# Performance work log

Measured on AMD Instinct MI355X. Metric: run time of the kernel, lower is better.

Reference implementation:

```python
import jax, jax.numpy as jnp
import numpy as np

NUM_HEADS = 8
EPS = 1e-12  # torch F.normalize eps


def _l2norm(t):
    # F.normalize(t, dim=-1): t / max(||t||, eps)
    n = jnp.sqrt(jnp.sum(t * t, axis=-1, keepdims=True))
    return t / jnp.maximum(n, EPS)


def setup_inputs() -> dict:
    key = jax.random.key(0)
    ks = jax.random.split(key, 4)
    B, C, H, W = 16, 384, 32, 32
    x = jax.random.normal(ks[0], (B, C, H, W), dtype=jnp.float32)
    temperature = jnp.ones((NUM_HEADS, 1, 1), dtype=jnp.float32)
    qkv_w = jax.random.normal(ks[1], (3 * C, C), dtype=jnp.float32) * (1.0 / np.sqrt(C))
    qkv_b = jnp.zeros((3 * C,), dtype=jnp.float32)
    proj_w = jax.random.normal(ks[2], (C, C), dtype=jnp.float32) * (1.0 / np.sqrt(C))
    proj_b = jnp.zeros((C,), dtype=jnp.float32)
    return {"x": x, "temperature": temperature, "qkv_w": qkv_w,
            "qkv_b": qkv_b, "proj_w": proj_w, "proj_b": proj_b}


def reference(x, temperature, qkv_w, qkv_b, proj_w, proj_b):
    B, C, H, W = x.shape
    nH = NUM_HEADS
    hd = C // nH
    N = H * W
    x_flat = x.reshape(B, C, N).transpose(0, 2, 1)            # [B, N, C]
    qkv = x_flat @ qkv_w.T + qkv_b                             # [B, N, 3C]
    qkv = qkv.reshape(B, N, 3, nH, hd).transpose(2, 0, 3, 1, 4)  # [3, B, nH, N, hd]
    q, k, v = qkv[0], qkv[1], qkv[2]
    q = _l2norm(q)
    k = _l2norm(k)
    attn = jnp.einsum('bhnd,bhmd->bhnm', q, k) * temperature   # [B, nH, N, N]
    attn = jax.nn.softmax(attn, axis=-1)
    out = jnp.einsum('bhnm,bhmd->bhnd', attn, v)               # [B, nH, N, hd]
    out = out.transpose(0, 2, 1, 3).reshape(B, N, C)           # [B, N, C]
    out = out @ proj_w.T + proj_b
    return out.transpose(0, 2, 1).reshape(B, C, H, W)
```

## Files before the change

kernel.cpp:

```cpp
#include <hip/hip_runtime.h>
#include <hip/hip_bf16.h>

#define Bb   16
#define Cc   384
#define Nn   1024
#define NH   8
#define HD   48
#define C3   1152
#define D64  64

typedef _Float16 f16x8 __attribute__((ext_vector_type(8)));
typedef __fp16   h16x2 __attribute__((ext_vector_type(2)));
typedef float    f32x4 __attribute__((ext_vector_type(4)));
typedef unsigned short ushort8 __attribute__((ext_vector_type(8)));

__device__ inline unsigned short f2h(float f) {
  union { _Float16 h; unsigned short u; } cv;
  cv.h = (_Float16)f;
  return cv.u;
}
__device__ inline unsigned int pk2u(float a, float b) {
  union { h16x2 v; unsigned int u; } cv;
  cv.v = __builtin_amdgcn_cvt_pkrtz(a, b);
  return cv.u;
}
__device__ inline void plswap(unsigned int &a, unsigned int &b) {
  asm("v_permlane16_swap_b32 %0, %1" : "+v"(a), "+v"(b));
}
__device__ inline f16x8 mk8(unsigned int a, unsigned int b,
                            unsigned int c, unsigned int d) {
  union { unsigned int u[4]; f16x8 h; } cv;
  cv.u[0] = a; cv.u[1] = b; cv.u[2] = c; cv.u[3] = d;
  return cv.h;
}

__device__ inline void gload_lds16(const unsigned short* g, unsigned short* l) {
  __builtin_amdgcn_global_load_lds(
      (const __attribute__((address_space(1))) void*)g,
      (__attribute__((address_space(3))) void*)l, 16, 0, 0);
}

__global__ __launch_bounds__(256) void prep_xsplit_kernel(
    const float* __restrict__ qkv_w, const float* __restrict__ pw,
    const float* __restrict__ x,
    unsigned short* __restrict__ wqh, unsigned short* __restrict__ pwh,
    unsigned short* __restrict__ vt, unsigned short* __restrict__ xh) {
  __shared__ float tile[64][65];
  const int bid = blockIdx.x;
  if (bid < 1728) {
    int i = bid * 256 + threadIdx.x;
    wqh[i] = f2h(qkv_w[i]);
  } else if (bid < 2304) {
    int i = (bid - 1728) * 256 + threadIdx.x;
    pwh[i] = f2h(pw[i]);
  } else if (bid < 3328) {
    int idx8 = (bid - 2304) * 256 + threadIdx.x;
    int bh = idx8 >> 11;
    int rem = idx8 & 2047;
    int row = 48 + (rem >> 7);
    int col = (rem & 127) * 8;
    unsigned short fill = (row == 48) ? (unsigned short)0x3C00 : (unsigned short)0;
    ushort8 v;
#pragma unroll
    for (int j = 0; j < 8; j++) v[j] = fill;
    *(ushort8*)(vt + (size_t)bh * D64 * Nn + (size_t)row * Nn + col) = v;
  } else {
    const int xb = bid - 3328;
    const int b  = xb / 96;
    const int rem = xb % 96;
    const int c0 = (rem / 16) * 64;
    const int n0 = (rem % 16) * 64;
    const int t  = threadIdx.x;
    const int rl = t >> 2, sc = (t & 3) * 16;
    {
      const float* src = x + ((size_t)b * Cc + c0 + rl) * Nn + n0 + sc;
#pragma unroll
      for (int i = 0; i < 4; i++) {
        float4 v = *(const float4*)(src + i * 4);
        tile[rl][sc + i * 4 + 0] = v.x; tile[rl][sc + i * 4 + 1] = v.y;
        tile[rl][sc + i * 4 + 2] = v.z; tile[rl][sc + i * 4 + 3] = v.w;
      }
    }
    __syncthreads();
    {
      ushort8 h0, h1;
#pragma unroll
      for (int i = 0; i < 8; i++) h0[i] = f2h(tile[sc + i][rl]);
#pragma unroll
      for (int i = 0; i < 8; i++) h1[i] = f2h(tile[sc + 8 + i][rl]);
      size_t dst = ((size_t)b * Nn + n0 + rl) * Cc + c0 + sc;
      *(ushort8*)(xh + dst) = h0; *(ushort8*)(xh + dst + 8) = h1;
    }
  }
}

__global__ __launch_bounds__(256, 4) void qkv_mfma(
    const unsigned short* __restrict__ wh,
    const unsigned short* __restrict__ xh,
    const float* __restrict__ bias, const float* __restrict__ temp,
    unsigned short* __restrict__ qh, unsigned short* __restrict__ kh,
    unsigned short* __restrict__ vt) {
  __shared__ unsigned short lds[128 * 136];
  unsigned short* Ash = lds;
  unsigned short* Bsh = lds + 6144;

  const int b  = blockIdx.z;
  const int yb = blockIdx.y;
  const int j0 = yb * 96;
  const int n0 = blockIdx.x * 128;
  const int tid = threadIdx.x;
  const int wave = tid >> 6, lane = tid & 63;
  const int quad = lane >> 4, l16 = lane & 15;
  const int wm = (wave >> 1) * 48, wn = (wave & 1) * 64;
  const int hs = wave >> 1;

  f32x4 acc[3][4];
#pragma unroll
  for (int mi = 0; mi < 3; mi++)
#pragma unroll
    for (int ni = 0; ni < 4; ni++) acc[mi][ni] = (f32x4){0.f, 0.f, 0.f, 0.f};

  const int sw = l16 & 7;

  for (int c0 = 0; c0 < Cc; c0 += 64) {
    __syncthreads();
#pragma unroll
    for (int s = 0; s < 3; s++) {
      int r  = s * 32 + wave * 8 + (lane >> 3);
      int cg = ((lane & 7) ^ (lane >> 3)) * 8;
      gload_lds16(wh + (size_t)(j0 + r) * Cc + c0 + cg,
                  &Ash[(s * 32 + wave * 8) * 64]);
    }
#pragma unroll
    for (int s = 0; s < 4; s++) {
      int r  = s * 32 + wave * 8 + (lane >> 3);
      int cg = ((lane & 7) ^ (lane >> 3)) * 8;
      gload_lds16(xh + ((size_t)b * Nn + n0 + r) * Cc + c0 + cg,
                  &Bsh[(s * 32 + wave * 8) * 64]);
    }
    __syncthreads();

#pragma unroll
    for (int ks = 0; ks < 64; ks += 32) {
      const int ach = (((ks >> 3) + quad) ^ sw) * 8;
      f16x8 ah[3], bh[4];
#pragma unroll
      for (int mi = 0; mi < 3; mi++)
        ah[mi] = *(const f16x8*)&Ash[(wm + mi * 16 + l16) * 64 + ach];
#pragma unroll
      for (int ni = 0; ni < 4; ni++)
        bh[ni] = *(const f16x8*)&Bsh[(wn + ni * 16 + l16) * 64 + ach];
#pragma unroll
      for (int mi = 0; mi < 3; mi++)
#pragma unroll
        for (int ni = 0; ni < 4; ni++)
          acc[mi][ni] = __builtin_amdgcn_mfma_f32_16x16x32_f16(ah[mi], bh[ni], acc[mi][ni], 0, 0, 0);
    }
  }

  const int part = yb >> 2;
  const int tq   = yb & 3;
  float bv[3][4];
#pragma unroll
  for (int mi = 0; mi < 3; mi++)
#pragma unroll
    for (int r = 0; r < 4; r++)
      bv[mi][r] = bias[j0 + wm + mi * 16 + quad * 4 + r];

  if (part < 2) {
    unsigned short* dst = part ? kh : qh;
    const float tmul = part ? 1.0f : temp[2 * tq + hs] * 1.44269504f;
    __syncthreads();
#pragma unroll
    for (int ni = 0; ni < 4; ni++) {
      float vals[3][4];
      float ss = 0.f;
#pragma unroll
      for (int mi = 0; mi < 3; mi++)
#pragma unroll
        for (int r = 0; r < 4; r++) {
          float v = acc[mi][ni][r] + bv[mi][r];
          vals[mi][r] = v; ss += v * v;
        }
      ss += __shfl_xor(ss, 16);
      ss += __shfl_xor(ss, 32);
      float scale = tmul / fmaxf(sqrtf(ss), 1e-12f);
      int n = wn + ni * 16 + l16;
#pragma unroll
      for (int mi = 0; mi < 3; mi++) {
        ushort4 sv;
        sv.x = f2h(vals[mi][0] * scale);
        sv.y = f2h(vals[mi][1] * scale);
        sv.z = f2h(vals[mi][2] * scale);
        sv.w = f2h(vals[mi][3] * scale);
        *(ushort4*)&lds[n * 136 + hs * 64 + mi * 16 + quad * 4] = sv;
      }
    }
    {
      int n = tid >> 1, h2 = tid & 1;
      ushort8 z = {0, 0, 0, 0, 0, 0, 0, 0};
      *(ushort8*)&lds[n * 136 + h2 * 64 + 48] = z;
      *(ushort8*)&lds[n * 136 + h2 * 64 + 56] = z;
    }
    __syncthreads();
#pragma unroll
    for (int it = 0; it < 8; it++) {
      int n = wave * 32 + it * 4 + (lane >> 4);
      int chunk = lane & 15;
      int hs3 = chunk >> 3, c8 = (chunk & 7) * 8;
      int h = 2 * tq + hs3;
      ushort8 v = *(const ushort8*)&lds[n * 136 + hs3 * 64 + c8];
      *(ushort8*)(dst + ((size_t)(b * NH + h) * Nn + n0 + n) * D64 + c8) = v;
    }
  } else {
    const int h = 2 * tq + hs;
#pragma unroll
    for (int mi = 0; mi < 3; mi++) {
#pragma unroll
      for (int r = 0; r < 4; r++) {
        int d = mi * 16 + quad * 4 + r;
        unsigned short* vrow = vt + ((size_t)(b * NH + h) * D64 + d) * Nn;
#pragma unroll
        for (int ni = 0; ni < 4; ni++) {
          int n = n0 + wn + ni * 16 + l16;
          vrow[n] = f2h(acc[mi][ni][r] + bv[mi][r]);
        }
      }
    }
  }
}

__global__ __launch_bounds__(256, 4) void attn_mfma(
    const unsigned short* __restrict__ qh, const unsigned short* __restrict__ kh,
    const unsigned short* __restrict__ vt,
    unsigned short* __restrict__ obh) {
  __shared__ __align__(16) unsigned short Kt[2][64 * 64];
  __shared__ __align__(16) unsigned short Vt[2][64 * 64];

  const int bid = blockIdx.x;
  const int hb = bid & 127;
  const int q0 = (bid >> 7) * 128;
  const int b = hb >> 3, h = hb & 7;
  const int tid = threadIdx.x;
  const int wave = tid >> 6, lane = tid & 63;
  const int quad = lane >> 4, l16 = lane & 15;
  const int qsw = ((quad & 1) << 1) | (quad >> 1);
  const int sx = (l16 & 7) * 8;

  const size_t headQ = ((size_t)(b * NH + h) * Nn) * D64;
  const unsigned short* Qg = qh + headQ + (size_t)(q0 + wave * 32) * D64;
  const unsigned short* Kg = kh + headQ;
  const unsigned short* Vg = vt + ((size_t)(b * NH + h) * D64) * Nn;

  f16x8 qa0[2], qa1[2];
#pragma unroll
  for (int m = 0; m < 2; m++) {
    qa0[m] = *(const f16x8*)(Qg + (m * 16 + l16) * D64 + quad * 8);
    qa1[m] = *(const f16x8*)(Qg + (m * 16 + l16) * D64 + quad * 8 + 32);
  }

  f32x4 oacc[2][4];
#pragma unroll
  for (int m = 0; m < 2; m++)
#pragma unroll
    for (int g = 0; g < 4; g++) oacc[m][g] = (f32x4){0.f, 0.f, 0.f, 0.f};
  const f32x4 zf = (f32x4){0.f, 0.f, 0.f, 0.f};

  const int srow = lane >> 3;
  const int scol = ((lane & 7) ^ srow) * 8;
  const int r0 = wave * 16;
  const unsigned short* KgS = Kg + (size_t)(r0 + srow) * D64 + scol;
  const unsigned short* VgS = Vg + (size_t)(r0 + srow) * Nn + scol;

  gload_lds16(KgS,           &Kt[0][r0 * 64]);
  gload_lds16(KgS + 8 * D64, &Kt[0][(r0 + 8) * 64]);
  gload_lds16(VgS,           &Vt[0][r0 * 64]);
  gload_lds16(VgS + 8 * Nn,  &Vt[0][(r0 + 8) * 64]);

  for (int kt = 0; kt < Nn / 64; kt++) {
    __syncthreads();
    const int cur = kt & 1;
    if (kt < Nn / 64 - 1) {
      const unsigned short* kn = KgS + (size_t)(kt + 1) * 64 * D64;
      const unsigned short* vn = VgS + (size_t)(kt + 1) * 64;
      gload_lds16(kn,           &Kt[cur ^ 1][r0 * 64]);
      gload_lds16(kn + 8 * D64, &Kt[cur ^ 1][(r0 + 8) * 64]);
      gload_lds16(vn,           &Vt[cur ^ 1][r0 * 64]);
      gload_lds16(vn + 8 * Nn,  &Vt[cur ^ 1][(r0 + 8) * 64]);
    }
    const unsigned short* Kl = Kt[cur];
    const unsigned short* Vl = Vt[cur];

    f32x4 sT[2][4];
    __builtin_amdgcn_s_setprio(1);
#pragma unroll
    for (int g = 0; g < 4; g++) {
      const unsigned short* kb = Kl + (g * 16 + l16) * 64;
      const int go = (quad * 8) ^ sx;
      f16x8 kf0 = *(const f16x8*)&kb[go];
      f16x8 kf1 = *(const f16x8*)&kb[go ^ 32];
#pragma unroll
      for (int m = 0; m < 2; m++) {
        f32x4 s = __builtin_amdgcn_mfma_f32_16x16x32_f16(kf0, qa0[m], zf, 0, 0, 0);
        sT[m][g] = __builtin_amdgcn_mfma_f32_16x16x32_f16(kf1, qa1[m], s, 0, 0, 0);
      }
    }
    __builtin_amdgcn_s_setprio(0);

    unsigned int w0[2][4], w1[2][4];
#pragma unroll
    for (int m = 0; m < 2; m++)
#pragma unroll
      for (int g = 0; g < 4; g++) {
        float e0 = __builtin_amdgcn_exp2f(sT[m][g][0]);
        float e1 = __builtin_amdgcn_exp2f(sT[m][g][1]);
        float e2 = __builtin_amdgcn_exp2f(sT[m][g][2]);
        float e3 = __builtin_amdgcn_exp2f(sT[m][g][3]);
        w0[m][g] = pk2u(e0, e1);
        w1[m][g] = pk2u(e2, e3);
      }

    f16x8 pa[2][2];
#pragma unroll
    for (int m = 0; m < 2; m++) {
      plswap(w0[m][0], w0[m][1]);
      plswap(w1[m][0], w1[m][1]);
      plswap(w0[m][2], w0[m][3]);
      plswap(w1[m][2], w1[m][3]);
      pa[m][0] = mk8(w0[m][0], w1[m][0], w0[m][1], w1[m][1]);
      pa[m][1] = mk8(w0[m][2], w1[m][2], w0[m][3], w1[m][3]);
    }

    __builtin_amdgcn_s_setprio(1);
#pragma unroll
    for (int g = 0; g < 4; g++) {
      const unsigned short* vb = Vl + (g * 16 + l16) * 64;
      const int go = (qsw * 8) ^ sx;
      f16x8 vf0 = *(const f16x8*)&vb[go];
      f16x8 vf1 = *(const f16x8*)&vb[go ^ 32];
#pragma unroll
      for (int m = 0; m < 2; m++) {
        oacc[m][g] = __builtin_amdgcn_mfma_f32_16x16x32_f16(vf0, pa[m][0], oacc[m][g], 0, 0, 0);
        oacc[m][g] = __builtin_amdgcn_mfma_f32_16x16x32_f16(vf1, pa[m][1], oacc[m][g], 0, 0, 0);
      }
    }
    __builtin_amdgcn_s_setprio(0);
  }

#pragma unroll
  for (int m = 0; m < 2; m++) {
    float inv = __builtin_amdgcn_rcpf(__shfl(oacc[m][3][0], l16));
    size_t obase = ((size_t)b * Nn + q0 + wave * 32 + m * 16 + l16) * Cc + h * HD;
#pragma unroll
    for (int g = 0; g < 3; g++) {
      ushort4 sv;
      sv.x = f2h(oacc[m][g][0] * inv);
      sv.y = f2h(oacc[m][g][1] * inv);
      sv.z = f2h(oacc[m][g][2] * inv);
      sv.w = f2h(oacc[m][g][3] * inv);
      *(ushort4*)(obh + obase + g * 16 + quad * 4) = sv;
    }
  }
}

__global__ __launch_bounds__(256, 4) void proj_mfma(
    const unsigned short* __restrict__ pwh,
    const unsigned short* __restrict__ obh,
    const float* __restrict__ pb, float* __restrict__ out) {
  __shared__ unsigned short Ash[128 * 64];
  __shared__ unsigned short Bsh[128 * 64];
  const int b  = blockIdx.z;
  const int c0m = blockIdx.y * 128;
  const int n0 = blockIdx.x * 128;
  const int tid = threadIdx.x;
  const int wave = tid >> 6, lane = tid & 63;
  const int quad = lane >> 4, l16 = lane & 15;
  const int wm = (wave >> 1) * 64, wn = (wave & 1) * 64;

  f32x4 acc[4][4];
#pragma unroll
  for (int mi = 0; mi < 4; mi++)
#pragma unroll
    for (int ni = 0; ni < 4; ni++) acc[mi][ni] = (f32x4){0.f, 0.f, 0.f, 0.f};

  const int sw = l16 & 7;

  for (int j0 = 0; j0 < Cc; j0 += 64) {
    __syncthreads();
#pragma unroll
    for (int s = 0; s < 4; s++) {
      int r  = s * 32 + wave * 8 + (lane >> 3);
      int cg = ((lane & 7) ^ (lane >> 3)) * 8;
      gload_lds16(pwh + (size_t)(c0m + r) * Cc + j0 + cg,
                  &Ash[(s * 32 + wave * 8) * 64]);
      gload_lds16(obh + ((size_t)b * Nn + n0 + r) * Cc + j0 + cg,
                  &Bsh[(s * 32 + wave * 8) * 64]);
    }
    __syncthreads();

#pragma unroll
    for (int ks = 0; ks < 64; ks += 32) {
      const int ach = (((ks >> 3) + quad) ^ sw) * 8;
      f16x8 ah[4], bh[4];
#pragma unroll
      for (int mi = 0; mi < 4; mi++)
        ah[mi] = *(const f16x8*)&Ash[(wm + mi * 16 + l16) * 64 + ach];
#pragma unroll
      for (int ni = 0; ni < 4; ni++)
        bh[ni] = *(const f16x8*)&Bsh[(wn + ni * 16 + l16) * 64 + ach];
#pragma unroll
      for (int mi = 0; mi < 4; mi++)
#pragma unroll
        for (int ni = 0; ni < 4; ni++)
          acc[mi][ni] = __builtin_amdgcn_mfma_f32_16x16x32_f16(ah[mi], bh[ni], acc[mi][ni], 0, 0, 0);
    }
  }

#pragma unroll
  for (int mi = 0; mi < 4; mi++) {
#pragma unroll
    for (int r = 0; r < 4; r++) {
      int c = c0m + wm + mi * 16 + quad * 4 + r;
      float bvv = pb[c];
#pragma unroll
      for (int ni = 0; ni < 4; ni++) {
        int n = n0 + wn + ni * 16 + l16;
        out[((size_t)b * Cc + c) * Nn + n] = acc[mi][ni][r] + bvv;
      }
    }
  }
}

extern "C" void kernel_launch(void* const* d_in, const int* in_sizes, int n_in,
                              void* d_out, int out_size, void* d_ws, size_t ws_size,
                              hipStream_t stream) {
  const float* x     = (const float*)d_in[0];
  const float* temp  = (const float*)d_in[1];
  const float* qkv_w = (const float*)d_in[2];
  const float* qkv_b = (const float*)d_in[3];
  const float* pw    = (const float*)d_in[4];
  const float* pb    = (const float*)d_in[5];
  float* out = (float*)d_out;

  const size_t QKN = (size_t)Bb * NH * Nn * D64;
  const size_t WQN = (size_t)C3 * Cc;
  const size_t PWN = (size_t)Cc * Cc;

  unsigned short* Qh  = (unsigned short*)d_ws;
  unsigned short* Kh  = Qh + QKN;
  unsigned short* VhT = Kh + QKN;
  unsigned short* Wqh = VhT + QKN;
  unsigned short* Pwh = Wqh + WQN;
  unsigned short* Xth = Pwh + PWN;
  unsigned short* Obh = Xth;

  prep_xsplit_kernel<<<4864, 256, 0, stream>>>(qkv_w, pw, x, Wqh, Pwh, VhT, Xth);
  qkv_mfma<<<dim3(Nn / 128, C3 / 96, Bb), 256, 0, stream>>>(Wqh, Xth, qkv_b, temp, Qh, Kh, VhT);
  attn_mfma<<<1024, 256, 0, stream>>>(Qh, Kh, VhT, Obh);
  proj_mfma<<<dim3(Nn / 128, Cc / 128, Bb), 256, 0, stream>>>(Pwh, Obh, pb, out);
}
```

Measured before the change: 156.0 us.

## Triple-buffer K/V tiles in attention with prefetch distance two and partial vmcnt waits

The attention kernel moves from double to triple buffering of the K and V LDS tiles and prefetches two tiles ahead. It replaces the blanket __syncthreads with an explicit s_waitcnt vmcnt(4) plus barrier, so the loads for the next tile can stay in flight. The aim is to hide global-to-LDS latency better. In exchange LDS use per block grows and launch bounds drop from 4 to 3 blocks per CU, which may lower occupancy.

```diff
diff --git a/kernel.cpp b/kernel.cpp
--- a/kernel.cpp
+++ b/kernel.cpp
@@ -230,12 +230,12 @@
   }
 }
 
-__global__ __launch_bounds__(256, 4) void attn_mfma(
+__global__ __launch_bounds__(256, 3) void attn_mfma(
     const unsigned short* __restrict__ qh, const unsigned short* __restrict__ kh,
     const unsigned short* __restrict__ vt,
     unsigned short* __restrict__ obh) {
-  __shared__ __align__(16) unsigned short Kt[2][64 * 64];
-  __shared__ __align__(16) unsigned short Vt[2][64 * 64];
+  __shared__ __align__(16) unsigned short Kt[3][64 * 64];
+  __shared__ __align__(16) unsigned short Vt[3][64 * 64];
 
   const int bid = blockIdx.x;
   const int hb = bid & 127;
@@ -272,21 +272,31 @@
   const unsigned short* KgS = Kg + (size_t)(r0 + srow) * D64 + scol;
   const unsigned short* VgS = Vg + (size_t)(r0 + srow) * Nn + scol;
 
-  gload_lds16(KgS,           &Kt[0][r0 * 64]);
-  gload_lds16(KgS + 8 * D64, &Kt[0][(r0 + 8) * 64]);
-  gload_lds16(VgS,           &Vt[0][r0 * 64]);
-  gload_lds16(VgS + 8 * Nn,  &Vt[0][(r0 + 8) * 64]);
-
+#pragma unroll
+  for (int t = 0; t < 2; t++) {
+    const unsigned short* kn = KgS + (size_t)t * 64 * D64;
+    const unsigned short* vn = VgS + (size_t)t * 64;
+    gload_lds16(kn,           &Kt[t][r0 * 64]);
+    gload_lds16(kn + 8 * D64, &Kt[t][(r0 + 8) * 64]);
+    gload_lds16(vn,           &Vt[t][r0 * 64]);
+    gload_lds16(vn + 8 * Nn,  &Vt[t][(r0 + 8) * 64]);
+  }
+
+  int cur = 0;
   for (int kt = 0; kt < Nn / 64; kt++) {
-    __syncthreads();
-    const int cur = kt & 1;
-    if (kt < Nn / 64 - 1) {
-      const unsigned short* kn = KgS + (size_t)(kt + 1) * 64 * D64;
-      const unsigned short* vn = VgS + (size_t)(kt + 1) * 64;
-      gload_lds16(kn,           &Kt[cur ^ 1][r0 * 64]);
-      gload_lds16(kn + 8 * D64, &Kt[cur ^ 1][(r0 + 8) * 64]);
-      gload_lds16(vn,           &Vt[cur ^ 1][r0 * 64]);
-      gload_lds16(vn + 8 * Nn,  &Vt[cur ^ 1][(r0 + 8) * 64]);
+    if (kt < Nn / 64 - 1) asm volatile("s_waitcnt vmcnt(4)" ::: "memory");
+    else                  asm volatile("s_waitcnt vmcnt(0)" ::: "memory");
+    __builtin_amdgcn_s_barrier();
+    asm volatile("" ::: "memory");
+
+    if (kt + 2 < Nn / 64) {
+      int nb = cur + 2 - ((cur + 2 >= 3) ? 3 : 0);
+      const unsigned short* kn = KgS + (size_t)(kt + 2) * 64 * D64;
+      const unsigned short* vn = VgS + (size_t)(kt + 2) * 64;
+      gload_lds16(kn,           &Kt[nb][r0 * 64]);
+      gload_lds16(kn + 8 * D64, &Kt[nb][(r0 + 8) * 64]);
+      gload_lds16(vn,           &Vt[nb][r0 * 64]);
+      gload_lds16(vn + 8 * Nn,  &Vt[nb][(r0 + 8) * 64]);
     }
     const unsigned short* Kl = Kt[cur];
     const unsigned short* Vl = Vt[cur];
@@ -345,6 +355,8 @@
       }
     }
     __builtin_amdgcn_s_setprio(0);
+
+    cur = cur + 1 - ((cur + 1 >= 3) ? 3 : 0);
   }
 
 #pragma unroll
```

New measurement: 164.7 us. 1.06x slower.
